# Performance work log

Hardware: AMD Instinct MI355X
Metric: run time of the kernel (lower is better)

Reference implementation:

```python
import jax, jax.numpy as jnp
import numpy as np

N_NODES = 100000
N_EDGES = 3200000
D_IN = 256
D_HID = 256
N_CLASS = 40


def setup_inputs() -> dict:
    key = jax.random.key(0)
    ks = jax.random.split(key, 8)
    x = jax.random.normal(ks[0], (N_NODES, D_IN), dtype=jnp.float32)
    edge_index = jax.random.randint(ks[1], (2, N_EDGES), 0, N_NODES, dtype=jnp.int64)
    s1 = 1.0 / np.sqrt(D_IN)
    s2 = 1.0 / np.sqrt(D_HID)
    W1_l = jax.random.normal(ks[2], (D_IN, D_HID), dtype=jnp.float32) * s1
    W1_r = jax.random.normal(ks[3], (D_IN, D_HID), dtype=jnp.float32) * s1
    b1 = jnp.zeros((D_HID,), dtype=jnp.float32)
    W2_l = jax.random.normal(ks[4], (D_HID, N_CLASS), dtype=jnp.float32) * s2
    W2_r = jax.random.normal(ks[5], (D_HID, N_CLASS), dtype=jnp.float32) * s2
    b2 = jnp.zeros((N_CLASS,), dtype=jnp.float32)
    return {"x": x, "edge_index": edge_index, "W1_l": W1_l, "W1_r": W1_r,
            "b1": b1, "W2_l": W2_l, "W2_r": W2_r, "b2": b2}


def _sage_conv(h, src, dst, deg_inv, Wl, Wr, b):
    # mean-aggregate source features into targets, then linear transforms
    agg = jax.ops.segment_sum(h[src], dst, num_segments=N_NODES)  # [N, d]
    agg = agg * deg_inv[:, None]
    return agg @ Wl + h @ Wr + b


def reference(x, edge_index, W1_l, W1_r, b1, W2_l, W2_r, b2):
    src, dst = edge_index[0], edge_index[1]
    deg = jax.ops.segment_sum(jnp.ones((src.shape[0],), dtype=x.dtype), dst,
                              num_segments=N_NODES)
    deg_inv = 1.0 / jnp.maximum(deg, 1.0)
    h = jax.nn.relu(_sage_conv(x, src, dst, deg_inv, W1_l, W1_r, b1))
    out = _sage_conv(h, src, dst, deg_inv, W2_l, W2_r, b2)
    return jax.nn.log_softmax(out, axis=1)
```

## Files before the change

kernel.cpp:

```cpp
#include <hip/hip_runtime.h>
#include <hip/hip_bf16.h>

#define THREADS 256
#define NB_MAX 400

typedef __attribute__((ext_vector_type(8))) short bf16x8;
typedef __attribute__((ext_vector_type(4))) float f32x4;
typedef __attribute__((ext_vector_type(2))) float f32x2;

__device__ __forceinline__ unsigned short f2b(float f) {
    __hip_bfloat16 h = __float2bfloat16(f);
    return *reinterpret_cast<unsigned short*>(&h);
}
__device__ __forceinline__ float b2f_lo(unsigned u) {
    unsigned v = u << 16;
    return __builtin_bit_cast(float, v);
}
__device__ __forceinline__ float b2f_hi(unsigned u) {
    unsigned v = u & 0xffff0000u;
    return __builtin_bit_cast(float, v);
}
__device__ __forceinline__ void gload_lds16(const void* g, void* l) {
    __builtin_amdgcn_global_load_lds(
        (const __attribute__((address_space(1))) void*)g,
        (__attribute__((address_space(3))) void*)l, 16, 0, 0);
}

__global__ __launch_bounds__(256) void k_hist(const int* __restrict__ dst, int E, int nbk,
                                              int* __restrict__ gcnt) {
    __shared__ int lc[NB_MAX];
    const int tid = threadIdx.x;
    for (int i = tid; i < nbk; i += 256) lc[i] = 0;
    __syncthreads();
    const int stride = gridDim.x * 256;
    for (int e = blockIdx.x * 256 + tid; e < E; e += stride)
        atomicAdd(&lc[dst[e] >> 8], 1);
    __syncthreads();
    for (int i = tid; i < nbk; i += 256)
        if (lc[i]) atomicAdd(&gcnt[i], lc[i]);
}

__global__ __launch_bounds__(512) void k_scanb(const int* __restrict__ gcnt, int* __restrict__ bptr,
                                               int* __restrict__ gcur, int nbk, int E) {
    __shared__ int sm[512];
    const int t = threadIdx.x;
    int v = (t < nbk) ? gcnt[t] : 0;
    sm[t] = v; __syncthreads();
    for (int off = 1; off < 512; off <<= 1) {
        int u = (t >= off) ? sm[t - off] : 0; __syncthreads();
        sm[t] += u; __syncthreads();
    }
    if (t < nbk) {
        int ex = sm[t] - v;
        bptr[t] = ex;
        gcur[t] = ex;
    }
    if (t == 0) bptr[nbk] = E;
}

__global__ __launch_bounds__(256) void k_bucket_scatter(const int* __restrict__ src, const int* __restrict__ dst,
                                                        int* __restrict__ gcur, unsigned* __restrict__ pairs,
                                                        int E, int nbk) {
    __shared__ int cnt[NB_MAX];
    __shared__ int base[NB_MAX];
    const int tid = threadIdx.x;
    const int e0 = blockIdx.x * 8192;
    for (int i = tid; i < nbk; i += 256) cnt[i] = 0;
    __syncthreads();
    #pragma unroll
    for (int j = 0; j < 32; ++j) {
        int e = e0 + j * 256 + tid;
        if (e < E) atomicAdd(&cnt[dst[e] >> 8], 1);
    }
    __syncthreads();
    for (int i = tid; i < nbk; i += 256)
        base[i] = cnt[i] ? atomicAdd(&gcur[i], cnt[i]) : 0;
    __syncthreads();
    #pragma unroll
    for (int j = 0; j < 32; ++j) {
        int e = e0 + j * 256 + tid;
        if (e < E) {
            int d = dst[e];
            int p = atomicAdd(&base[d >> 8], 1);
            pairs[p] = ((unsigned)src[e] << 8) | ((unsigned)d & 255u);
        }
    }
}

__global__ __launch_bounds__(256) void k_bucket_csr(const int* __restrict__ bptr, const unsigned* __restrict__ pairs,
                                                    int* __restrict__ rowptr, float* __restrict__ dinv,
                                                    int* __restrict__ csr_src, int N, int nbk, int E) {
    __shared__ int deg[256];
    __shared__ int sm[256];
    __shared__ int cur[256];
    const int b = blockIdx.x;
    const int tid = threadIdx.x;
    const int e0 = bptr[b], e1 = bptr[b + 1];

    deg[tid] = 0;
    __syncthreads();
    for (int e = e0 + tid; e < e1; e += 256)
        atomicAdd(&deg[pairs[e] & 255u], 1);
    __syncthreads();
    int d = deg[tid];
    sm[tid] = d; __syncthreads();
    for (int off = 1; off < 256; off <<= 1) {
        int u = (tid >= off) ? sm[tid - off] : 0; __syncthreads();
        sm[tid] += u; __syncthreads();
    }
    int ex = sm[tid] - d;
    int node = (b << 8) + tid;
    cur[tid] = e0 + ex;
    if (node < N) {
        rowptr[node] = e0 + ex;
        dinv[node] = 1.0f / (float)max(d, 1);
    }
    if (b == nbk - 1 && tid == 0) rowptr[N] = E;
    __syncthreads();
    for (int e = e0 + tid; e < e1; e += 256) {
        unsigned u = pairs[e];
        int p = atomicAdd(&cur[u & 255u], 1);
        csr_src[p] = (int)(u >> 8);
    }
}

__global__ __launch_bounds__(256) void k_cvtX(const float* __restrict__ x, unsigned short* __restrict__ xb,
                                              unsigned char* __restrict__ xq, int N, int Npad) {
    int i = blockIdx.x * THREADS + threadIdx.x;
    if (i >= Npad * 32) return;
    int row = i >> 5;
    unsigned short o[8];
    int q0 = 0, q1 = 0;
    if (row < N) {
        float4 v0 = reinterpret_cast<const float4*>(x)[2 * (size_t)i];
        float4 v1 = reinterpret_cast<const float4*>(x)[2 * (size_t)i + 1];
        o[0] = f2b(v0.x); o[1] = f2b(v0.y); o[2] = f2b(v0.z); o[3] = f2b(v0.w);
        o[4] = f2b(v1.x); o[5] = f2b(v1.y); o[6] = f2b(v1.z); o[7] = f2b(v1.w);
        q0 = __builtin_amdgcn_cvt_pk_fp8_f32(v0.x, v0.y, q0, false);
        q0 = __builtin_amdgcn_cvt_pk_fp8_f32(v0.z, v0.w, q0, true);
        q1 = __builtin_amdgcn_cvt_pk_fp8_f32(v1.x, v1.y, q1, false);
        q1 = __builtin_amdgcn_cvt_pk_fp8_f32(v1.z, v1.w, q1, true);
    } else {
        #pragma unroll
        for (int j = 0; j < 8; ++j) o[j] = 0;
    }
    reinterpret_cast<uint4*>(xb)[i] = *reinterpret_cast<uint4*>(o);
    reinterpret_cast<uint2*>(xq)[i] = make_uint2((unsigned)q0, (unsigned)q1);
}

__global__ __launch_bounds__(256) void k_cvtW(const float* __restrict__ W1l, const float* __restrict__ W1r,
                                              unsigned short* __restrict__ WbT) {
    int idx = blockIdx.x * THREADS + threadIdx.x;
    if (idx >= 256 * 512) return;
    int n = idx >> 9, k = idx & 511;
    float v = (k < 256) ? W1l[(size_t)k * 256 + n] : W1r[(size_t)(k - 256) * 256 + n];
    WbT[idx] = f2b(v);
}

__global__ __launch_bounds__(256) void k_cvtW2(const float* __restrict__ W2l, const float* __restrict__ W2r,
                                               unsigned short* __restrict__ WbT2) {
    int idx = blockIdx.x * THREADS + threadIdx.x;
    if (idx >= 80 * 256) return;
    int n = idx >> 8, k = idx & 255;
    float v = (n < 40) ? W2l[(size_t)k * 40 + n] : W2r[(size_t)k * 40 + (n - 40)];
    WbT2[idx] = f2b(v);
}

__global__ __launch_bounds__(256) void k_agg1(const int* __restrict__ rowptr, const int* __restrict__ csr_src,
                                              const float* __restrict__ dinv, const unsigned char* __restrict__ xq,
                                              unsigned short* __restrict__ aggb, int N, int Npad) {
    int gid = blockIdx.x * THREADS + threadIdx.x;
    int node = gid >> 5, lane = gid & 31;
    if (node >= N) {
        if (node < Npad)
            reinterpret_cast<uint4*>(aggb + (size_t)node * 256 + lane * 8)[0] = make_uint4(0, 0, 0, 0);
        return;
    }
    const int e0 = rowptr[node], e1 = rowptr[node + 1];
    const unsigned char* xl = xq + (size_t)lane * 8;
    float acc[8] = {};
    for (int eb = e0; eb < e1; eb += 32) {
        int n = min(32, e1 - eb);
        int sidx = (eb + lane < e1) ? csr_src[eb + lane] : 0;
        int j = 0;
        for (; j + 7 < n; j += 8) {
            uint2 vv[8];
            #pragma unroll
            for (int q = 0; q < 8; ++q) {
                int s = __shfl(sidx, j + q, 32);
                vv[q] = *reinterpret_cast<const uint2*>(xl + (size_t)s * 256);
            }
            #pragma unroll
            for (int q = 0; q < 8; ++q) {
                f32x2 p0 = __builtin_amdgcn_cvt_pk_f32_fp8((int)vv[q].x, false);
                f32x2 p1 = __builtin_amdgcn_cvt_pk_f32_fp8((int)vv[q].x, true);
                f32x2 p2 = __builtin_amdgcn_cvt_pk_f32_fp8((int)vv[q].y, false);
                f32x2 p3 = __builtin_amdgcn_cvt_pk_f32_fp8((int)vv[q].y, true);
                acc[0] += p0.x; acc[1] += p0.y;
                acc[2] += p1.x; acc[3] += p1.y;
                acc[4] += p2.x; acc[5] += p2.y;
                acc[6] += p3.x; acc[7] += p3.y;
            }
        }
        for (; j < n; ++j) {
            int s = __shfl(sidx, j, 32);
            uint2 v = *reinterpret_cast<const uint2*>(xl + (size_t)s * 256);
            f32x2 p0 = __builtin_amdgcn_cvt_pk_f32_fp8((int)v.x, false);
            f32x2 p1 = __builtin_amdgcn_cvt_pk_f32_fp8((int)v.x, true);
            f32x2 p2 = __builtin_amdgcn_cvt_pk_f32_fp8((int)v.y, false);
            f32x2 p3 = __builtin_amdgcn_cvt_pk_f32_fp8((int)v.y, true);
            acc[0] += p0.x; acc[1] += p0.y;
            acc[2] += p1.x; acc[3] += p1.y;
            acc[4] += p2.x; acc[5] += p2.y;
            acc[6] += p3.x; acc[7] += p3.y;
        }
    }
    const float ds = dinv[node];
    unsigned short o[8];
    #pragma unroll
    for (int j = 0; j < 8; ++j) o[j] = f2b(acc[j] * ds);
    *reinterpret_cast<uint4*>(aggb + (size_t)node * 256 + lane * 8) = *reinterpret_cast<uint4*>(o);
}

__global__ __launch_bounds__(512) void k_gemm1(
    const unsigned short* __restrict__ aggb, const unsigned short* __restrict__ xb,
    const unsigned short* __restrict__ WbT, const float* __restrict__ b1,
    unsigned short* __restrict__ hb, int M)
{
    __shared__ unsigned short As[128 * 64];
    __shared__ unsigned short Bs[256 * 64];

    const int tid  = threadIdx.x;
    const int lane = tid & 63;
    const int wave = tid >> 6;
    const int row0 = blockIdx.x * 128;
    const int wm0  = (wave >> 2) * 64;
    const int wn0  = (wave & 3) * 64;

    const int ldr = lane >> 3;
    const int lsw = ((lane & 7) ^ ldr) * 8;

    f32x4 acc[4][4];
    #pragma unroll
    for (int m = 0; m < 4; ++m)
        #pragma unroll
        for (int n = 0; n < 4; ++n)
            acc[m][n] = (f32x4){0.f, 0.f, 0.f, 0.f};

    for (int kt = 0; kt < 8; ++kt) {
        const unsigned short* Abase = (kt < 4) ? aggb : xb;
        const int kcol = (kt & 3) * 64;
        __syncthreads();
        #pragma unroll
        for (int i = 0; i < 2; ++i) {
            const int c = wave * 2 + i;
            const unsigned short* ga = Abase + (size_t)(row0 + c * 8 + ldr) * 256 + kcol + lsw;
            gload_lds16(ga, &As[c * 512]);
        }
        #pragma unroll
        for (int i = 0; i < 4; ++i) {
            const int c = wave * 4 + i;
            const unsigned short* gb = WbT + (size_t)(c * 8 + ldr) * 512 + kt * 64 + lsw;
            gload_lds16(gb, &Bs[c * 512]);
        }
        __syncthreads();
        #pragma unroll
        for (int kk = 0; kk < 2; ++kk) {
            bf16x8 af[4], bf[4];
            #pragma unroll
            for (int m = 0; m < 4; ++m) {
                const int r = wm0 + m * 16 + (lane & 15);
                const int s = (kk * 4 + (lane >> 4)) ^ (r & 7);
                af[m] = *reinterpret_cast<const bf16x8*>(&As[r * 64 + s * 8]);
            }
            #pragma unroll
            for (int n = 0; n < 4; ++n) {
                const int r = wn0 + n * 16 + (lane & 15);
                const int s = (kk * 4 + (lane >> 4)) ^ (r & 7);
                bf[n] = *reinterpret_cast<const bf16x8*>(&Bs[r * 64 + s * 8]);
            }
            #pragma unroll
            for (int m = 0; m < 4; ++m)
                #pragma unroll
                for (int n = 0; n < 4; ++n)
                    acc[m][n] = __builtin_amdgcn_mfma_f32_16x16x32_bf16(af[m], bf[n], acc[m][n], 0, 0, 0);
        }
    }

    const int crow = (lane >> 4) * 4;
    const int ccol = lane & 15;
    #pragma unroll
    for (int n = 0; n < 4; ++n) {
        const int col = wn0 + n * 16 + ccol;
        const float bias = b1[col];
        #pragma unroll
        for (int m = 0; m < 4; ++m) {
            const int rbase = row0 + wm0 + m * 16 + crow;
            #pragma unroll
            for (int r = 0; r < 4; ++r) {
                const int row = rbase + r;
                if (row < M) {
                    float v = fmaxf(acc[m][n][r] + bias, 0.f);
                    hb[(size_t)row * 256 + col] = f2b(v);
                }
            }
        }
    }
}

__global__ __launch_bounds__(256) void k_gemm2(
    const unsigned short* __restrict__ hb, const unsigned short* __restrict__ WbT2,
    const float* __restrict__ b2,
    unsigned char* __restrict__ Tq, float* __restrict__ Up, int M)
{
    __shared__ unsigned short As[128 * 64];
    __shared__ unsigned short Bs2[80 * 264];

    const int tid  = threadIdx.x;
    const int lane = tid & 63;
    const int wave = tid >> 6;
    const int row0 = blockIdx.x * 128;

    const int ldr = lane >> 3;
    const int lsw = ((lane & 7) ^ ldr) * 8;

    for (int idx = tid; idx < 80 * 32; idx += 256) {
        int row = idx >> 5, un = idx & 31;
        uint4 d = *reinterpret_cast<const uint4*>(WbT2 + (size_t)row * 256 + un * 8);
        *reinterpret_cast<uint4*>(&Bs2[row * 264 + un * 8]) = d;
    }

    f32x4 acc[2][5];
    #pragma unroll
    for (int m = 0; m < 2; ++m)
        #pragma unroll
        for (int n = 0; n < 5; ++n)
            acc[m][n] = (f32x4){0.f, 0.f, 0.f, 0.f};

    for (int kt = 0; kt < 4; ++kt) {
        __syncthreads();
        #pragma unroll
        for (int i = 0; i < 4; ++i) {
            const int c = wave * 4 + i;
            const unsigned short* ga = hb + (size_t)(row0 + c * 8 + ldr) * 256 + kt * 64 + lsw;
            gload_lds16(ga, &As[c * 512]);
        }
        __syncthreads();
        #pragma unroll
        for (int kk = 0; kk < 2; ++kk) {
            bf16x8 af[2], bf[5];
            #pragma unroll
            for (int m = 0; m < 2; ++m) {
                const int r = wave * 32 + m * 16 + (lane & 15);
                const int s = (kk * 4 + (lane >> 4)) ^ (r & 7);
                af[m] = *reinterpret_cast<const bf16x8*>(&As[(r & 127) * 64 + s * 8]);
            }
            #pragma unroll
            for (int n = 0; n < 5; ++n) {
                const int r = n * 16 + (lane & 15);
                bf[n] = *reinterpret_cast<const bf16x8*>(&Bs2[r * 264 + kt * 64 + kk * 32 + (lane >> 4) * 8]);
            }
            #pragma unroll
            for (int m = 0; m < 2; ++m)
                #pragma unroll
                for (int n = 0; n < 5; ++n)
                    acc[m][n] = __builtin_amdgcn_mfma_f32_16x16x32_bf16(af[m], bf[n], acc[m][n], 0, 0, 0);
        }
    }

    const int crow = (lane >> 4) * 4;
    const int ccol = lane & 15;
    #pragma unroll
    for (int n = 0; n < 5; ++n) {
        const int col = n * 16 + ccol;
        #pragma unroll
        for (int m = 0; m < 2; ++m) {
            const int rbase = row0 + wave * 32 + m * 16 + crow;
            #pragma unroll
            for (int r = 0; r < 4; ++r) {
                const int row = rbase + r;
                if (row < M) {
                    float v = acc[m][n][r];
                    if (col < 40) {
                        int q = __builtin_amdgcn_cvt_pk_fp8_f32(v, v, 0, false);
                        Tq[(size_t)row * 40 + col] = (unsigned char)(q & 0xff);
                    } else {
                        Up[(size_t)row * 40 + (col - 40)] = v + b2[col - 40];
                    }
                }
            }
        }
    }
}

__global__ __launch_bounds__(256) void k_final(const int* __restrict__ rowptr, const int* __restrict__ csr_src,
                                               const float* __restrict__ dinv, const unsigned char* __restrict__ Tq,
                                               const float* __restrict__ Up, float* __restrict__ out, int N) {
    int gid = blockIdx.x * THREADS + threadIdx.x;
    int node = gid >> 6, lane = gid & 63;
    if (node >= N) return;
    const int e0 = rowptr[node], e1 = rowptr[node + 1];
    const int g = lane / 10;
    const int c = lane % 10;
    float a0 = 0.f, a1 = 0.f, a2 = 0.f, a3 = 0.f;
    for (int eb = e0; eb < e1; eb += 64) {
        int sidx = (eb + lane < e1) ? csr_src[eb + lane] : 0;
        int nn = min(64, e1 - eb);
        for (int jb = 0; jb < nn; jb += 6) {
            int ei = jb + g;
            bool valid = (g < 6) && (ei < nn);
            int s = __shfl(sidx, ei & 63, 64);
            if (valid) {
                unsigned u = *reinterpret_cast<const unsigned*>(Tq + (size_t)s * 40 + c * 4);
                f32x2 lo = __builtin_amdgcn_cvt_pk_f32_fp8((int)u, false);
                f32x2 hi = __builtin_amdgcn_cvt_pk_f32_fp8((int)u, true);
                a0 += lo.x; a1 += lo.y;
                a2 += hi.x; a3 += hi.y;
            }
        }
    }
    float t0 = a0, t1 = a1, t2 = a2, t3 = a3;
    #pragma unroll
    for (int gg = 1; gg < 6; ++gg) {
        t0 += __shfl(a0, c + 10 * gg, 64);
        t1 += __shfl(a1, c + 10 * gg, 64);
        t2 += __shfl(a2, c + 10 * gg, 64);
        t3 += __shfl(a3, c + 10 * gg, 64);
    }
    float v0 = -1e30f, v1 = -1e30f, v2 = -1e30f, v3 = -1e30f;
    if (lane < 10) {
        const float ds = dinv[node];
        float4 up = *reinterpret_cast<const float4*>(Up + (size_t)node * 40 + lane * 4);
        v0 = t0 * ds + up.x; v1 = t1 * ds + up.y;
        v2 = t2 * ds + up.z; v3 = t3 * ds + up.w;
    }
    float m = fmaxf(fmaxf(v0, v1), fmaxf(v2, v3));
    #pragma unroll
    for (int o = 8; o > 0; o >>= 1) m = fmaxf(m, __shfl_xor(m, o, 16));
    float e = 0.f;
    if (lane < 10) e = expf(v0 - m) + expf(v1 - m) + expf(v2 - m) + expf(v3 - m);
    float ssum = e;
    #pragma unroll
    for (int o = 8; o > 0; o >>= 1) ssum += __shfl_xor(ssum, o, 16);
    float ls = logf(ssum);
    if (lane < 10) {
        float4 o4;
        o4.x = v0 - m - ls; o4.y = v1 - m - ls;
        o4.z = v2 - m - ls; o4.w = v3 - m - ls;
        *reinterpret_cast<float4*>(out + (size_t)node * 40 + lane * 4) = o4;
    }
}

extern "C" void kernel_launch(void* const* d_in, const int* in_sizes, int n_in,
                              void* d_out, int out_size, void* d_ws, size_t ws_size,
                              hipStream_t stream) {
    const float* x   = (const float*)d_in[0];
    const int*   ei  = (const int*)d_in[1];
    const float* W1l = (const float*)d_in[2];
    const float* W1r = (const float*)d_in[3];
    const float* b1  = (const float*)d_in[4];
    const float* W2l = (const float*)d_in[5];
    const float* W2r = (const float*)d_in[6];
    const float* b2  = (const float*)d_in[7];
    float* out = (float*)d_out;

    const int N = in_sizes[0] / 256;
    const int E = in_sizes[1] / 2;
    const int Npad = ((N + 127) / 128) * 128;
    const int nbk = (N + 255) / 256;
    const int* src = ei;
    const int* dst = ei + E;

    char* ws = (char*)d_ws;
    size_t off = 0;
    int*   gcnt    = (int*)(ws + off); off += (size_t)NB_MAX * 4;
    int*   bptr    = (int*)(ws + off); off += (size_t)(NB_MAX + 1) * 4;
    int*   gcur    = (int*)(ws + off); off += (size_t)NB_MAX * 4;
    int*   rowptr  = (int*)(ws + off); off += (size_t)(N + 1) * 4;
    float* dinv    = (float*)(ws + off); off += (size_t)N * 4;
    off = (off + 255) & ~(size_t)255;
    unsigned* pairs = (unsigned*)(ws + off); off += (size_t)E * 4;
    int*   csr_src = (int*)(ws + off); off += (size_t)E * 4;
    off = (off + 255) & ~(size_t)255;
    unsigned short* xb   = (unsigned short*)(ws + off); off += (size_t)Npad * 256 * 2;
    unsigned char*  xq   = (unsigned char*)(ws + off);  off += (size_t)Npad * 256;
    unsigned short* aggb = (unsigned short*)(ws + off); off += (size_t)Npad * 256 * 2;
    unsigned short* hb   = (unsigned short*)(ws + off); off += (size_t)Npad * 256 * 2;
    unsigned short* WbT  = (unsigned short*)(ws + off); off += (size_t)256 * 512 * 2;
    unsigned short* WbT2 = (unsigned short*)(ws + off); off += (size_t)80 * 256 * 2;
    off = (off + 255) & ~(size_t)255;
    unsigned char* Tq    = (unsigned char*)(ws + off);  off += (size_t)Npad * 40;
    off = (off + 255) & ~(size_t)255;
    float*          Up   = (float*)(ws + off);          off += (size_t)Npad * 40 * 4;

    hipMemsetAsync(gcnt, 0, (size_t)NB_MAX * 4, stream);

    const int nsb = (E + 8191) / 8192;
    k_hist<<<nsb, THREADS, 0, stream>>>(dst, E, nbk, gcnt);
    k_scanb<<<1, 512, 0, stream>>>(gcnt, bptr, gcur, nbk, E);
    k_bucket_scatter<<<nsb, THREADS, 0, stream>>>(src, dst, gcur, pairs, E, nbk);
    k_bucket_csr<<<nbk, THREADS, 0, stream>>>(bptr, pairs, rowptr, dinv, csr_src, N, nbk, E);

    k_cvtX<<<(Npad * 32 + THREADS - 1) / THREADS, THREADS, 0, stream>>>(x, xb, xq, N, Npad);
    k_cvtW<<<(256 * 512 + THREADS - 1) / THREADS, THREADS, 0, stream>>>(W1l, W1r, WbT);
    k_cvtW2<<<(80 * 256 + THREADS - 1) / THREADS, THREADS, 0, stream>>>(W2l, W2r, WbT2);

    k_agg1<<<(Npad * 32 + THREADS - 1) / THREADS, THREADS, 0, stream>>>(rowptr, csr_src, dinv, xq, aggb, N, Npad);

    k_gemm1<<<Npad / 128, 512, 0, stream>>>(aggb, xb, WbT, b1, hb, N);

    k_gemm2<<<Npad / 128, THREADS, 0, stream>>>(hb, WbT2, b2, Tq, Up, N);

    k_final<<<((size_t)N * 64 + THREADS - 1) / THREADS, THREADS, 0, stream>>>(rowptr, csr_src, dinv, Tq, Up, out, N);
}
```

Measured before the change: 407.4 us.

## Sort CSR neighbours by source range and merge conversion kernels

The CSR build now sub-buckets each destination's edges into 13 source-index ranges, so neighbour lists are ordered roughly by source id. This should make the gathers in the aggregation kernels more cache-friendly. The three conversion kernels are merged into one launch, and the fp8 accumulation now uses packed float2 adds. The cost is 13 KB more shared memory per CSR block and an extra prefix pass.

```diff
diff --git a/kernel.cpp b/kernel.cpp
--- a/kernel.cpp
+++ b/kernel.cpp
@@ -3,6 +3,7 @@
 
 #define THREADS 256
 #define NB_MAX 400
+#define NPH 13
 
 typedef __attribute__((ext_vector_type(8))) short bf16x8;
 typedef __attribute__((ext_vector_type(4))) float f32x4;
@@ -12,13 +13,9 @@
     __hip_bfloat16 h = __float2bfloat16(f);
     return *reinterpret_cast<unsigned short*>(&h);
 }
-__device__ __forceinline__ float b2f_lo(unsigned u) {
-    unsigned v = u << 16;
-    return __builtin_bit_cast(float, v);
-}
-__device__ __forceinline__ float b2f_hi(unsigned u) {
-    unsigned v = u & 0xffff0000u;
-    return __builtin_bit_cast(float, v);
+__device__ __forceinline__ unsigned char f2q(float v) {
+    int q = __builtin_amdgcn_cvt_pk_fp8_f32(v, v, 0, false);
+    return (unsigned char)(q & 0xff);
 }
 __device__ __forceinline__ void gload_lds16(const void* g, void* l) {
     __builtin_amdgcn_global_load_lds(
@@ -90,19 +87,33 @@
 __global__ __launch_bounds__(256) void k_bucket_csr(const int* __restrict__ bptr, const unsigned* __restrict__ pairs,
                                                     int* __restrict__ rowptr, float* __restrict__ dinv,
                                                     int* __restrict__ csr_src, int N, int nbk, int E) {
+    __shared__ int pc[256 * NPH];
     __shared__ int deg[256];
     __shared__ int sm[256];
-    __shared__ int cur[256];
+    __shared__ int nodebase[256];
     const int b = blockIdx.x;
     const int tid = threadIdx.x;
     const int e0 = bptr[b], e1 = bptr[b + 1];
 
-    deg[tid] = 0;
-    __syncthreads();
-    for (int e = e0 + tid; e < e1; e += 256)
-        atomicAdd(&deg[pairs[e] & 255u], 1);
-    __syncthreads();
-    int d = deg[tid];
+    #pragma unroll
+    for (int i = 0; i < NPH; ++i) pc[i * 256 + tid] = 0;
+    __syncthreads();
+    for (int e = e0 + tid; e < e1; e += 256) {
+        unsigned u = pairs[e];
+        int n = (int)(u & 255u);
+        int ph = (int)(u >> 8) >> 13;
+        atomicAdd(&pc[ph * 256 + n], 1);
+    }
+    __syncthreads();
+    int run = 0;
+    #pragma unroll
+    for (int ph = 0; ph < NPH; ++ph) {
+        int c = pc[ph * 256 + tid];
+        pc[ph * 256 + tid] = run;
+        run += c;
+    }
+    int d = run;
+    deg[tid] = d;
     sm[tid] = d; __syncthreads();
     for (int off = 1; off < 256; off <<= 1) {
         int u = (tid >= off) ? sm[tid - off] : 0; __syncthreads();
@@ -110,60 +121,65 @@
     }
     int ex = sm[tid] - d;
     int node = (b << 8) + tid;
-    cur[tid] = e0 + ex;
+    int nb_ = e0 + ex;
+    nodebase[tid] = nb_;
     if (node < N) {
-        rowptr[node] = e0 + ex;
+        rowptr[node] = nb_;
         dinv[node] = 1.0f / (float)max(d, 1);
     }
     if (b == nbk - 1 && tid == 0) rowptr[N] = E;
+    __syncthreads();
+    #pragma unroll
+    for (int ph = 0; ph < NPH; ++ph) pc[ph * 256 + tid] += nodebase[tid];
     __syncthreads();
     for (int e = e0 + tid; e < e1; e += 256) {
         unsigned u = pairs[e];
-        int p = atomicAdd(&cur[u & 255u], 1);
-        csr_src[p] = (int)(u >> 8);
-    }
-}
-
-__global__ __launch_bounds__(256) void k_cvtX(const float* __restrict__ x, unsigned short* __restrict__ xb,
-                                              unsigned char* __restrict__ xq, int N, int Npad) {
+        int n = (int)(u & 255u);
+        int s = (int)(u >> 8);
+        int p = atomicAdd(&pc[(s >> 13) * 256 + n], 1);
+        csr_src[p] = s;
+    }
+}
+
+__global__ __launch_bounds__(256) void k_cvt(const float* __restrict__ x, unsigned short* __restrict__ xb,
+                                             unsigned char* __restrict__ xq, int N, int Npad,
+                                             const float* __restrict__ W1l, const float* __restrict__ W1r,
+                                             const float* __restrict__ W2l, const float* __restrict__ W2r,
+                                             unsigned short* __restrict__ WbT, unsigned short* __restrict__ WbT2) {
     int i = blockIdx.x * THREADS + threadIdx.x;
-    if (i >= Npad * 32) return;
-    int row = i >> 5;
-    unsigned short o[8];
-    int q0 = 0, q1 = 0;
-    if (row < N) {
-        float4 v0 = reinterpret_cast<const float4*>(x)[2 * (size_t)i];
-        float4 v1 = reinterpret_cast<const float4*>(x)[2 * (size_t)i + 1];
-        o[0] = f2b(v0.x); o[1] = f2b(v0.y); o[2] = f2b(v0.z); o[3] = f2b(v0.w);
-        o[4] = f2b(v1.x); o[5] = f2b(v1.y); o[6] = f2b(v1.z); o[7] = f2b(v1.w);
-        q0 = __builtin_amdgcn_cvt_pk_fp8_f32(v0.x, v0.y, q0, false);
-        q0 = __builtin_amdgcn_cvt_pk_fp8_f32(v0.z, v0.w, q0, true);
-        q1 = __builtin_amdgcn_cvt_pk_fp8_f32(v1.x, v1.y, q1, false);
-        q1 = __builtin_amdgcn_cvt_pk_fp8_f32(v1.z, v1.w, q1, true);
-    } else {
-        #pragma unroll
-        for (int j = 0; j < 8; ++j) o[j] = 0;
-    }
-    reinterpret_cast<uint4*>(xb)[i] = *reinterpret_cast<uint4*>(o);
-    reinterpret_cast<uint2*>(xq)[i] = make_uint2((unsigned)q0, (unsigned)q1);
-}
-
-__global__ __launch_bounds__(256) void k_cvtW(const float* __restrict__ W1l, const float* __restrict__ W1r,
-                                              unsigned short* __restrict__ WbT) {
-    int idx = blockIdx.x * THREADS + threadIdx.x;
-    if (idx >= 256 * 512) return;
-    int n = idx >> 9, k = idx & 511;
-    float v = (k < 256) ? W1l[(size_t)k * 256 + n] : W1r[(size_t)(k - 256) * 256 + n];
-    WbT[idx] = f2b(v);
-}
-
-__global__ __launch_bounds__(256) void k_cvtW2(const float* __restrict__ W2l, const float* __restrict__ W2r,
-                                               unsigned short* __restrict__ WbT2) {
-    int idx = blockIdx.x * THREADS + threadIdx.x;
-    if (idx >= 80 * 256) return;
-    int n = idx >> 8, k = idx & 255;
-    float v = (n < 40) ? W2l[(size_t)k * 40 + n] : W2r[(size_t)k * 40 + (n - 40)];
-    WbT2[idx] = f2b(v);
+    const int nxu = Npad * 32;
+    if (i < nxu) {
+        int row = i >> 5;
+        unsigned short o[8];
+        int q0 = 0, q1 = 0;
+        if (row < N) {
+            float4 v0 = reinterpret_cast<const float4*>(x)[2 * (size_t)i];
+            float4 v1 = reinterpret_cast<const float4*>(x)[2 * (size_t)i + 1];
+            o[0] = f2b(v0.x); o[1] = f2b(v0.y); o[2] = f2b(v0.z); o[3] = f2b(v0.w);
+            o[4] = f2b(v1.x); o[5] = f2b(v1.y); o[6] = f2b(v1.z); o[7] = f2b(v1.w);
+            q0 = __builtin_amdgcn_cvt_pk_fp8_f32(v0.x, v0.y, q0, false);
+            q0 = __builtin_amdgcn_cvt_pk_fp8_f32(v0.z, v0.w, q0, true);
+            q1 = __builtin_amdgcn_cvt_pk_fp8_f32(v1.x, v1.y, q1, false);
+            q1 = __builtin_amdgcn_cvt_pk_fp8_f32(v1.z, v1.w, q1, true);
+        } else {
+            #pragma unroll
+            for (int j = 0; j < 8; ++j) o[j] = 0;
+        }
+        reinterpret_cast<uint4*>(xb)[i] = *reinterpret_cast<uint4*>(o);
+        reinterpret_cast<uint2*>(xq)[i] = make_uint2((unsigned)q0, (unsigned)q1);
+        return;
+    }
+    int idx = i - nxu;
+    if (idx < 131072) {
+        int n = idx >> 9, k = idx & 511;
+        float v = (k < 256) ? W1l[(size_t)k * 256 + n] : W1r[(size_t)(k - 256) * 256 + n];
+        WbT[idx] = f2b(v);
+    } else if (idx < 131072 + 20480) {
+        int j = idx - 131072;
+        int n = j >> 8, k = j & 255;
+        float v = (n < 40) ? W2l[(size_t)k * 40 + n] : W2r[(size_t)k * 40 + (n - 40)];
+        WbT2[j] = f2b(v);
+    }
 }
 
 __global__ __launch_bounds__(256) void k_agg1(const int* __restrict__ rowptr, const int* __restrict__ csr_src,
@@ -178,7 +194,9 @@
     }
     const int e0 = rowptr[node], e1 = rowptr[node + 1];
     const unsigned char* xl = xq + (size_t)lane * 8;
-    float acc[8] = {};
+    f32x2 acc[4];
+    #pragma unroll
+    for (int j = 0; j < 4; ++j) acc[j] = (f32x2){0.f, 0.f};
     for (int eb = e0; eb < e1; eb += 32) {
         int n = min(32, e1 - eb);
         int sidx = (eb + lane < e1) ? csr_src[eb + lane] : 0;
@@ -192,33 +210,28 @@
             }
             #pragma unroll
             for (int q = 0; q < 8; ++q) {
-                f32x2 p0 = __builtin_amdgcn_cvt_pk_f32_fp8((int)vv[q].x, false);
-                f32x2 p1 = __builtin_amdgcn_cvt_pk_f32_fp8((int)vv[q].x, true);
-                f32x2 p2 = __builtin_amdgcn_cvt_pk_f32_fp8((int)vv[q].y, false);
-                f32x2 p3 = __builtin_amdgcn_cvt_pk_f32_fp8((int)vv[q].y, true);
-                acc[0] += p0.x; acc[1] += p0.y;
-                acc[2] += p1.x; acc[3] += p1.y;
-                acc[4] += p2.x; acc[5] += p2.y;
-                acc[6] += p3.x; acc[7] += p3.y;
+                acc[0] += __builtin_amdgcn_cvt_pk_f32_fp8((int)vv[q].x, false);
+                acc[1] += __builtin_amdgcn_cvt_pk_f32_fp8((int)vv[q].x, true);
+                acc[2] += __builtin_amdgcn_cvt_pk_f32_fp8((int)vv[q].y, false);
+                acc[3] += __builtin_amdgcn_cvt_pk_f32_fp8((int)vv[q].y, true);
             }
         }
         for (; j < n; ++j) {
             int s = __shfl(sidx, j, 32);
             uint2 v = *reinterpret_cast<const uint2*>(xl + (size_t)s * 256);
-            f32x2 p0 = __builtin_amdgcn_cvt_pk_f32_fp8((int)v.x, false);
-            f32x2 p1 = __builtin_amdgcn_cvt_pk_f32_fp8((int)v.x, true);
-            f32x2 p2 = __builtin_amdgcn_cvt_pk_f32_fp8((int)v.y, false);
-            f32x2 p3 = __builtin_amdgcn_cvt_pk_f32_fp8((int)v.y, true);
-            acc[0] += p0.x; acc[1] += p0.y;
-            acc[2] += p1.x; acc[3] += p1.y;
-            acc[4] += p2.x; acc[5] += p2.y;
-            acc[6] += p3.x; acc[7] += p3.y;
+            acc[0] += __builtin_amdgcn_cvt_pk_f32_fp8((int)v.x, false);
+            acc[1] += __builtin_amdgcn_cvt_pk_f32_fp8((int)v.x, true);
+            acc[2] += __builtin_amdgcn_cvt_pk_f32_fp8((int)v.y, false);
+            acc[3] += __builtin_amdgcn_cvt_pk_f32_fp8((int)v.y, true);
         }
     }
     const float ds = dinv[node];
     unsigned short o[8];
     #pragma unroll
-    for (int j = 0; j < 8; ++j) o[j] = f2b(acc[j] * ds);
+    for (int j = 0; j < 4; ++j) {
+        o[2 * j + 0] = f2b(acc[j].x * ds);
+        o[2 * j + 1] = f2b(acc[j].y * ds);
+    }
     *reinterpret_cast<uint4*>(aggb + (size_t)node * 256 + lane * 8) = *reinterpret_cast<uint4*>(o);
 }
 
@@ -381,12 +394,10 @@
                 const int row = rbase + r;
                 if (row < M) {
                     float v = acc[m][n][r];
-                    if (col < 40) {
-                        int q = __builtin_amdgcn_cvt_pk_fp8_f32(v, v, 0, false);
-                        Tq[(size_t)row * 40 + col] = (unsigned char)(q & 0xff);
-                    } else {
+                    if (col < 40)
+                        Tq[(size_t)row * 40 + col] = f2q(v);
+                    else
                         Up[(size_t)row * 40 + (col - 40)] = v + b2[col - 40];
-                    }
                 }
             }
         }
@@ -489,7 +500,7 @@
     unsigned short* WbT  = (unsigned short*)(ws + off); off += (size_t)256 * 512 * 2;
     unsigned short* WbT2 = (unsigned short*)(ws + off); off += (size_t)80 * 256 * 2;
     off = (off + 255) & ~(size_t)255;
-    unsigned char* Tq    = (unsigned char*)(ws + off);  off += (size_t)Npad * 40;
+    unsigned char*  Tq   = (unsigned char*)(ws + off);  off += (size_t)Npad * 40;
     off = (off + 255) & ~(size_t)255;
     float*          Up   = (float*)(ws + off);          off += (size_t)Npad * 40 * 4;
 
@@ -501,11 +512,11 @@
     k_bucket_scatter<<<nsb, THREADS, 0, stream>>>(src, dst, gcur, pairs, E, nbk);
     k_bucket_csr<<<nbk, THREADS, 0, stream>>>(bptr, pairs, rowptr, dinv, csr_src, N, nbk, E);
 
-    k_cvtX<<<(Npad * 32 + THREADS - 1) / THREADS, THREADS, 0, stream>>>(x, xb, xq, N, Npad);
-    k_cvtW<<<(256 * 512 + THREADS - 1) / THREADS, THREADS, 0, stream>>>(W1l, W1r, WbT);
-    k_cvtW2<<<(80 * 256 + THREADS - 1) / THREADS, THREADS, 0, stream>>>(W2l, W2r, WbT2);
-
-    k_agg1<<<(Npad * 32 + THREADS - 1) / THREADS, THREADS, 0, stream>>>(rowptr, csr_src, dinv, xq, aggb, N, Npad);
+    const int ncvt = Npad * 32 + 131072 + 20480;
+    k_cvt<<<(ncvt + THREADS - 1) / THREADS, THREADS, 0, stream>>>(x, xb, xq, N, Npad,
+                                                                  W1l, W1r, W2l, W2r, WbT, WbT2);
+
+    k_agg1<<<((size_t)Npad * 32 + THREADS - 1) / THREADS, THREADS, 0, stream>>>(rowptr, csr_src, dinv, xq, aggb, N, Npad);
 
     k_gemm1<<<Npad / 128, 512, 0, stream>>>(aggb, xb, WbT, b1, hb, N);
 
```

Result: no change. 401.4 us (-1.5%).
